# Optimization experiments

Hardware: AMD Instinct MI355X
Metric: run time of the kernel (lower is better)

The kernel has to match this reference:

```python
import jax, jax.numpy as jnp
import numpy as np

B, OBS, ACT, H, K = 32768, 64, 12, 256, 16
LOG_STD_MIN, LOG_STD_MAX = -10.0, 2.0


def setup_inputs() -> dict:
    key = jax.random.key(0)
    ks = jax.random.split(key, 9)
    s = lambda k, shape, scale: jax.random.normal(k, shape, jnp.float32) * scale
    return {
        "obs": jax.random.normal(ks[0], (B, OBS), jnp.float32),
        "idx": jax.random.randint(ks[1], (B,), 0, K),
        "noise": jax.random.normal(ks[2], (B, ACT), jnp.float32),
        "W1": s(ks[3], (OBS, H), 0.1), "b1": jnp.zeros((H,), jnp.float32),
        "W2": s(ks[4], (H, H), 0.05), "b2": jnp.zeros((H,), jnp.float32),
        "HW1": s(ks[5], (K, H, H), 0.05), "Hb1": jnp.zeros((K, H), jnp.float32),
        "HW2": s(ks[6], (K, H, 2 * ACT), 0.05), "Hb2": jnp.zeros((K, 2 * ACT), jnp.float32),
    }


def reference(obs, idx, noise, W1, b1, W2, b2, HW1, Hb1, HW2, Hb2):
    # Trunk MLP: Linear-ReLU-Linear, then the Sequential's extra ReLU.
    h = jax.nn.relu(obs @ W1 + b1)
    h = h @ W2 + b2
    h = jax.nn.relu(h)  # [B, H]
    # Per-head ensemble FFN computed densely for ALL heads (as in the original).
    y = jax.nn.relu(jnp.einsum('bh,khd->kbd', h, HW1) + Hb1[:, None, :])  # [K, B, H]
    out = jnp.einsum('kbd,kde->kbe', y, HW2) + Hb2[:, None, :]            # [K, B, 2A]
    # Top-1 per-sample head gather: out[idx, arange(B)]
    out = out[idx, jnp.arange(obs.shape[0])]                              # [B, 2A]
    A = out.shape[-1] // 2
    mean, log_std = out[:, :A], out[:, A:]
    # Bounded std via tanh
    log_std = LOG_STD_MIN + 0.5 * (LOG_STD_MAX - LOG_STD_MIN) * (jnp.tanh(log_std) + 1.0)
    std = jnp.exp(log_std)
    # rsample with explicit noise
    act = mean + std * noise
    # Normal log_prob
    logp = -0.5 * jnp.square((act - mean) / std) - log_std - 0.5 * jnp.log(2.0 * jnp.pi)
    # tanh squash with log-det correction
    sq = jnp.tanh(act)
    slogp = jnp.sum(logp - jnp.log(1.0 - jnp.square(sq) + 1e-6), axis=-1)  # [B]
    return sq, slogp
```

## Files before the change

### kernel.cpp

```cpp
#include <hip/hip_runtime.h>
#include <hip/hip_bf16.h>

typedef __bf16 bf16x8 __attribute__((ext_vector_type(8)));
typedef float  f32x4  __attribute__((ext_vector_type(4)));

#define MFMA16(a,b,c) __builtin_amdgcn_mfma_f32_16x16x32_bf16((a),(b),(c),0,0,0)

#define NB 32768

#define WS_COUNTS   0
#define WS_CURSORS  64
#define WS_TILEBASE 128
#define WS_BASES    256
#define WS_PERM     512
#define WS_W1P      131584
#define WS_W2P      164352
#define WS_HW1P     295424
#define WS_HW2P     2392576

__global__ void pack_kernel(const float* __restrict__ W1, const float* __restrict__ W2,
                            const float* __restrict__ HW1, const float* __restrict__ HW2,
                            char* __restrict__ ws) {
  if (blockIdx.x == 0 && threadIdx.x < 32)
    ((int*)ws)[threadIdx.x] = 0;
  int p = blockIdx.x * 256 + threadIdx.x;
  if (p < 16384) {
    int pp = p;
    int w = pp >> 12, r = pp & 4095;
    int f = r >> 9, e = r & 511;
    int lane = e >> 3, j = e & 7;
    int kt = f >> 2, nt = f & 3;
    int k = kt*32 + (lane>>4)*8 + j;
    int n = w*64 + nt*16 + (lane&15);
    ((__bf16*)(ws + WS_W1P))[pp] = (__bf16)W1[k*256 + n];
  } else if (p < 81920) {
    int pp = p - 16384;
    int w = pp >> 14, r = pp & 16383;
    int f = r >> 9, e = r & 511;
    int lane = e >> 3, j = e & 7;
    int kt = f >> 2, nt = f & 3;
    int k = kt*32 + (lane>>4)*8 + j;
    int n = w*64 + nt*16 + (lane&15);
    ((__bf16*)(ws + WS_W2P))[pp] = (__bf16)W2[k*256 + n];
  } else if (p < 1130496) {
    int p3 = p - 81920;
    int head = p3 >> 16, pp = p3 & 65535;
    int w = pp >> 14, r = pp & 16383;
    int f = r >> 9, e = r & 511;
    int lane = e >> 3, j = e & 7;
    int kt = f >> 2, nt = f & 3;
    int k = kt*32 + (lane>>4)*8 + j;
    int n = w*64 + nt*16 + (lane&15);
    ((__bf16*)(ws + WS_HW1P))[head*65536 + pp] = (__bf16)HW1[head*65536 + k*256 + n];
  } else if (p < 1261568) {
    int p4 = p - 1130496;
    int head = p4 >> 13, pp = p4 & 8191;
    int f = pp >> 9, e = pp & 511;
    int lane = e >> 3, j = e & 7;
    int kt = f >> 1, nt = f & 1;
    int k = kt*32 + (lane>>4)*8 + j;
    int n = nt*16 + (lane&15);
    __bf16 v = (__bf16)0.0f;
    if (n < 24) v = (__bf16)HW2[head*(256*24) + k*24 + n];
    ((__bf16*)(ws + WS_HW2P))[head*8192 + pp] = v;
  }
}

__global__ void hist_kernel(const int* __restrict__ idx, char* __restrict__ ws) {
  __shared__ int lc[16];
  int t = threadIdx.x;
  if (t < 16) lc[t] = 0;
  __syncthreads();
  int b = blockIdx.x * 256 + t;
  atomicAdd(&lc[idx[b]], 1);
  __syncthreads();
  if (t < 16 && lc[t]) atomicAdd(&((int*)(ws + WS_COUNTS))[t], lc[t]);
}

__global__ void scan_kernel(char* __restrict__ ws) {
  if (threadIdx.x == 0) {
    int* counts  = (int*)(ws + WS_COUNTS);
    int* cursors = (int*)(ws + WS_CURSORS);
    int* tb      = (int*)(ws + WS_TILEBASE);
    int* bases   = (int*)(ws + WS_BASES);
    int base = 0, tbase = 0;
    for (int k = 0; k < 16; k++) {
      bases[k] = base; cursors[k] = base; tb[k] = tbase;
      base  += counts[k];
      tbase += (counts[k] + 63) >> 6;
    }
    tb[16] = tbase;
  }
}

__global__ void scatter_kernel(const int* __restrict__ idx, char* __restrict__ ws) {
  __shared__ int lc[16], lbase[16];
  int t = threadIdx.x;
  if (t < 16) lc[t] = 0;
  __syncthreads();
  int b = blockIdx.x * 256 + t;
  int k = idx[b];
  int lp = atomicAdd(&lc[k], 1);
  __syncthreads();
  if (t < 16 && lc[t]) lbase[t] = atomicAdd(&((int*)(ws + WS_CURSORS))[t], lc[t]);
  __syncthreads();
  ((int*)(ws + WS_PERM))[lbase[k] + lp] = b;
}

__device__ __forceinline__ void gemm_relu(char* sA, const __bf16* __restrict__ Bp,
                                          const float* __restrict__ bias, int w, int l) {
  int q = l >> 4, l15 = l & 15;
  f32x4 zf = {0.f, 0.f, 0.f, 0.f};
  f32x4 acc[4][4];
#pragma unroll
  for (int mt = 0; mt < 4; mt++)
#pragma unroll
    for (int nt = 0; nt < 4; nt++) acc[mt][nt] = zf;
#pragma unroll
  for (int kt = 0; kt < 8; kt++) {
    bf16x8 af[4], bg[4];
#pragma unroll
    for (int mt = 0; mt < 4; mt++)
      af[mt] = *(const bf16x8*)(sA + (mt*16 + l15)*528 + (kt*32 + q*8)*2);
#pragma unroll
    for (int nt = 0; nt < 4; nt++)
      bg[nt] = *(const bf16x8*)(Bp + w*16384 + (kt*4 + nt)*512 + l*8);
#pragma unroll
    for (int mt = 0; mt < 4; mt++)
#pragma unroll
      for (int nt = 0; nt < 4; nt++)
        acc[mt][nt] = MFMA16(af[mt], bg[nt], acc[mt][nt]);
  }
  __syncthreads();
  float bv[4];
#pragma unroll
  for (int nt = 0; nt < 4; nt++) bv[nt] = bias[w*64 + nt*16 + l15];
#pragma unroll
  for (int mt = 0; mt < 4; mt++)
#pragma unroll
    for (int nt = 0; nt < 4; nt++)
#pragma unroll
      for (int r = 0; r < 4; r++) {
        float v = fmaxf(acc[mt][nt][r] + bv[nt], 0.f);
        int row = mt*16 + q*4 + r;
        int col = w*64 + nt*16 + l15;
        *(__bf16*)(sA + row*528 + col*2) = (__bf16)v;
      }
  __syncthreads();
}

__global__ __launch_bounds__(256, 2)
void actor_kernel(const float* __restrict__ obs, const float* __restrict__ noise,
                  const float* __restrict__ b1, const float* __restrict__ b2,
                  const float* __restrict__ Hb1, const float* __restrict__ Hb2,
                  const char* __restrict__ ws, float* __restrict__ out) {
  __shared__ __align__(16) char smem[43264];
  char*  sA    = smem;
  char*  sA0   = smem + 33792;
  float* souts = (float*)(smem + 33792);
  int*   rows  = (int*)(smem + 43008);

  const int* cnts  = (const int*)(ws + WS_COUNTS);
  const int* tb    = (const int*)(ws + WS_TILEBASE);
  const int* bases = (const int*)(ws + WS_BASES);
  const int* perm  = (const int*)(ws + WS_PERM);

  int bid = blockIdx.x;
  if (bid >= tb[16]) return;
  int head = 0;
#pragma unroll
  for (int k = 1; k < 16; k++) if (bid >= tb[k]) head = k;
  int row0  = bases[head] + (bid - tb[head]) * 64;
  int nrows = bases[head] + cnts[head] - row0;
  if (nrows > 64) nrows = 64;

  int t = threadIdx.x;
  int w = t >> 6, l = t & 63, q = l >> 4, l15 = l & 15;

  if (t < 64) rows[t] = (t < nrows) ? perm[row0 + t] : -1;
  __syncthreads();

  for (int s = t; s < 512; s += 256) {
    int m = s >> 3, c = (s & 7) << 3;
    int rm = rows[m];
    bf16x8 v = {};
    if (rm >= 0) {
#pragma unroll
      for (int i = 0; i < 8; i++) v[i] = (__bf16)obs[rm*64 + c + i];
    }
    *(bf16x8*)(sA0 + m*144 + c*2) = v;
  }
  __syncthreads();

  {
    const __bf16* Bp = (const __bf16*)(ws + WS_W1P) + w*4096;
    f32x4 zf = {0.f, 0.f, 0.f, 0.f};
    f32x4 acc[4][4];
#pragma unroll
    for (int mt = 0; mt < 4; mt++)
#pragma unroll
      for (int nt = 0; nt < 4; nt++) acc[mt][nt] = zf;
#pragma unroll
    for (int kt = 0; kt < 2; kt++) {
      bf16x8 af[4], bg[4];
#pragma unroll
      for (int mt = 0; mt < 4; mt++)
        af[mt] = *(const bf16x8*)(sA0 + (mt*16 + l15)*144 + (kt*32 + q*8)*2);
#pragma unroll
      for (int nt = 0; nt < 4; nt++)
        bg[nt] = *(const bf16x8*)(Bp + (kt*4 + nt)*512 + l*8);
#pragma unroll
      for (int mt = 0; mt < 4; mt++)
#pragma unroll
        for (int nt = 0; nt < 4; nt++)
          acc[mt][nt] = MFMA16(af[mt], bg[nt], acc[mt][nt]);
    }
    float bv[4];
#pragma unroll
    for (int nt = 0; nt < 4; nt++) bv[nt] = b1[w*64 + nt*16 + l15];
#pragma unroll
    for (int mt = 0; mt < 4; mt++)
#pragma unroll
      for (int nt = 0; nt < 4; nt++)
#pragma unroll
        for (int r = 0; r < 4; r++) {
          float v = fmaxf(acc[mt][nt][r] + bv[nt], 0.f);
          int row = mt*16 + q*4 + r;
          int col = w*64 + nt*16 + l15;
          *(__bf16*)(sA + row*528 + col*2) = (__bf16)v;
        }
  }
  __syncthreads();

  gemm_relu(sA, (const __bf16*)(ws + WS_W2P), b2, w, l);
  gemm_relu(sA, (const __bf16*)(ws + WS_HW1P) + head*65536, Hb1 + head*256, w, l);

  {
    const __bf16* Bp = (const __bf16*)(ws + WS_HW2P) + head*8192;
    f32x4 zf = {0.f, 0.f, 0.f, 0.f};
    f32x4 c4[2]; c4[0] = zf; c4[1] = zf;
#pragma unroll
    for (int kt = 0; kt < 8; kt++) {
      bf16x8 af = *(const bf16x8*)(sA + (w*16 + l15)*528 + (kt*32 + q*8)*2);
#pragma unroll
      for (int nt = 0; nt < 2; nt++) {
        bf16x8 bg = *(const bf16x8*)(Bp + (kt*2 + nt)*512 + l*8);
        c4[nt] = MFMA16(af, bg, c4[nt]);
      }
    }
    __syncthreads();
#pragma unroll
    for (int nt = 0; nt < 2; nt++)
#pragma unroll
      for (int r = 0; r < 4; r++) {
        int row = w*16 + q*4 + r;
        int col = nt*16 + l15;
        float v = c4[nt][r];
        if (col < 24) v += Hb2[head*24 + col];
        souts[row*32 + col] = v;
      }
  }
  __syncthreads();

  {
    int row = t >> 2, sub = t & 3;
    int bnum = (row < nrows) ? rows[row] : -1;
    float s = 0.f;
    if (bnum >= 0) {
#pragma unroll
      for (int i = 0; i < 3; i++) {
        int a = sub*3 + i;
        float mean = souts[row*32 + a];
        float lsr  = souts[row*32 + 12 + a];
        float ls   = -10.f + 6.f*(tanhf(lsr) + 1.f);
        float sd   = __expf(ls);
        float nz   = noise[bnum*12 + a];
        float act  = mean + sd*nz;
        float sq   = tanhf(act);
        out[bnum*12 + a] = sq;
        s += -0.5f*nz*nz - ls - 0.91893853320467274f - __logf(1.f - sq*sq + 1e-6f);
      }
    }
    s += __shfl_xor(s, 1);
    s += __shfl_xor(s, 2);
    if (bnum >= 0 && sub == 0) out[NB*12 + bnum] = s;
  }
}

extern "C" void kernel_launch(void* const* d_in, const int* in_sizes, int n_in,
                              void* d_out, int out_size, void* d_ws, size_t ws_size,
                              hipStream_t stream) {
  const float* obs   = (const float*)d_in[0];
  const int*   idx   = (const int*)d_in[1];
  const float* noise = (const float*)d_in[2];
  const float* W1    = (const float*)d_in[3];
  const float* b1    = (const float*)d_in[4];
  const float* W2    = (const float*)d_in[5];
  const float* b2    = (const float*)d_in[6];
  const float* HW1   = (const float*)d_in[7];
  const float* Hb1   = (const float*)d_in[8];
  const float* HW2   = (const float*)d_in[9];
  const float* Hb2   = (const float*)d_in[10];
  char* ws = (char*)d_ws;

  pack_kernel<<<4928, 256, 0, stream>>>(W1, W2, HW1, HW2, ws);
  hist_kernel<<<128, 256, 0, stream>>>(idx, ws);
  scan_kernel<<<1, 64, 0, stream>>>(ws);
  scatter_kernel<<<128, 256, 0, stream>>>(idx, ws);
  actor_kernel<<<528, 256, 0, stream>>>(obs, noise, b1, b2, Hb1, Hb2, ws, (float*)d_out);
}
```

Before: 108.4 us.

## Drop histogram and scan kernels via per-head bucket scatter; tile weight packing

Removes the hist and scan launches. Each head now gets a fixed-capacity bucket in the permutation buffer, and the scatter cursors serve directly as per-head counts, which the actor kernel reads to compute its tile-to-head mapping. The weight pack kernel is rewritten to stage 32-row slabs through shared memory with coalesced float4 reads and vectorized bf16x8 writes, using far fewer blocks. This costs a larger workspace of 16 buckets times 32768 ints and adds a 16-entry prefix loop in every actor block.

```diff
diff --git a/kernel.cpp b/kernel.cpp
--- a/kernel.cpp
+++ b/kernel.cpp
@@ -7,89 +7,67 @@
 #define MFMA16(a,b,c) __builtin_amdgcn_mfma_f32_16x16x32_bf16((a),(b),(c),0,0,0)
 
 #define NB 32768
-
-#define WS_COUNTS   0
+#define CAP 32768
+
 #define WS_CURSORS  64
-#define WS_TILEBASE 128
-#define WS_BASES    256
 #define WS_PERM     512
-#define WS_W1P      131584
-#define WS_W2P      164352
-#define WS_HW1P     295424
-#define WS_HW2P     2392576
-
-__global__ void pack_kernel(const float* __restrict__ W1, const float* __restrict__ W2,
-                            const float* __restrict__ HW1, const float* __restrict__ HW2,
-                            char* __restrict__ ws) {
-  if (blockIdx.x == 0 && threadIdx.x < 32)
-    ((int*)ws)[threadIdx.x] = 0;
-  int p = blockIdx.x * 256 + threadIdx.x;
-  if (p < 16384) {
-    int pp = p;
-    int w = pp >> 12, r = pp & 4095;
-    int f = r >> 9, e = r & 511;
-    int lane = e >> 3, j = e & 7;
-    int kt = f >> 2, nt = f & 3;
-    int k = kt*32 + (lane>>4)*8 + j;
-    int n = w*64 + nt*16 + (lane&15);
-    ((__bf16*)(ws + WS_W1P))[pp] = (__bf16)W1[k*256 + n];
-  } else if (p < 81920) {
-    int pp = p - 16384;
-    int w = pp >> 14, r = pp & 16383;
-    int f = r >> 9, e = r & 511;
-    int lane = e >> 3, j = e & 7;
-    int kt = f >> 2, nt = f & 3;
-    int k = kt*32 + (lane>>4)*8 + j;
-    int n = w*64 + nt*16 + (lane&15);
-    ((__bf16*)(ws + WS_W2P))[pp] = (__bf16)W2[k*256 + n];
-  } else if (p < 1130496) {
-    int p3 = p - 81920;
-    int head = p3 >> 16, pp = p3 & 65535;
-    int w = pp >> 14, r = pp & 16383;
-    int f = r >> 9, e = r & 511;
-    int lane = e >> 3, j = e & 7;
-    int kt = f >> 2, nt = f & 3;
-    int k = kt*32 + (lane>>4)*8 + j;
-    int n = w*64 + nt*16 + (lane&15);
-    ((__bf16*)(ws + WS_HW1P))[head*65536 + pp] = (__bf16)HW1[head*65536 + k*256 + n];
-  } else if (p < 1261568) {
-    int p4 = p - 1130496;
-    int head = p4 >> 13, pp = p4 & 8191;
-    int f = pp >> 9, e = pp & 511;
-    int lane = e >> 3, j = e & 7;
-    int kt = f >> 1, nt = f & 1;
-    int k = kt*32 + (lane>>4)*8 + j;
-    int n = nt*16 + (lane&15);
-    __bf16 v = (__bf16)0.0f;
-    if (n < 24) v = (__bf16)HW2[head*(256*24) + k*24 + n];
-    ((__bf16*)(ws + WS_HW2P))[head*8192 + pp] = v;
-  }
-}
-
-__global__ void hist_kernel(const int* __restrict__ idx, char* __restrict__ ws) {
-  __shared__ int lc[16];
-  int t = threadIdx.x;
-  if (t < 16) lc[t] = 0;
-  __syncthreads();
-  int b = blockIdx.x * 256 + t;
-  atomicAdd(&lc[idx[b]], 1);
-  __syncthreads();
-  if (t < 16 && lc[t]) atomicAdd(&((int*)(ws + WS_COUNTS))[t], lc[t]);
-}
-
-__global__ void scan_kernel(char* __restrict__ ws) {
-  if (threadIdx.x == 0) {
-    int* counts  = (int*)(ws + WS_COUNTS);
-    int* cursors = (int*)(ws + WS_CURSORS);
-    int* tb      = (int*)(ws + WS_TILEBASE);
-    int* bases   = (int*)(ws + WS_BASES);
-    int base = 0, tbase = 0;
-    for (int k = 0; k < 16; k++) {
-      bases[k] = base; cursors[k] = base; tb[k] = tbase;
-      base  += counts[k];
-      tbase += (counts[k] + 63) >> 6;
-    }
-    tb[16] = tbase;
+#define WS_W1P      2097664
+#define WS_W2P      2130432
+#define WS_HW1P     2261504
+#define WS_HW2P     4358656
+
+__global__ __launch_bounds__(256)
+void pack_kernel(const float* __restrict__ W1, const float* __restrict__ W2,
+                 const float* __restrict__ HW1, const float* __restrict__ HW2,
+                 char* __restrict__ ws) {
+  __shared__ __bf16 tile[32 * 260];
+  int b = blockIdx.x, t = threadIdx.x;
+  if (b == 0 && t < 32) ((int*)ws)[t] = 0;
+
+  const float* src; __bf16* dst; int kt, wstride, hw2 = 0;
+  if (b < 2)        { src = W1;  dst = (__bf16*)(ws + WS_W1P); kt = b;      wstride = 4096;  }
+  else if (b < 10)  { src = W2;  dst = (__bf16*)(ws + WS_W2P); kt = b - 2;  wstride = 16384; }
+  else if (b < 138) { int h = (b - 10) >> 3; kt = (b - 10) & 7;
+                      src = HW1 + h*65536; dst = (__bf16*)(ws + WS_HW1P) + h*65536; wstride = 16384; }
+  else              { int h = (b - 138) >> 3; kt = (b - 138) & 7;
+                      src = HW2 + h*6144;  dst = (__bf16*)(ws + WS_HW2P) + h*8192;  hw2 = 1; }
+
+  int wv = t >> 6, l = t & 63;
+  if (!hw2) {
+    const float4* s4 = (const float4*)(src + kt*32*256);
+#pragma unroll
+    for (int p = 0; p < 8; p++) {
+      int i = p*256 + t;
+      int rr = i >> 6, c4 = i & 63;
+      float4 v = s4[i];
+      __bf16* d = &tile[rr*260 + c4*4];
+      d[0] = (__bf16)v.x; d[1] = (__bf16)v.y; d[2] = (__bf16)v.z; d[3] = (__bf16)v.w;
+    }
+    __syncthreads();
+#pragma unroll
+    for (int nt = 0; nt < 4; nt++) {
+      bf16x8 v;
+#pragma unroll
+      for (int j = 0; j < 8; j++)
+        v[j] = tile[((l>>4)*8 + j)*260 + wv*64 + nt*16 + (l&15)];
+      *(bf16x8*)(dst + wv*wstride + (kt*4 + nt)*512 + l*8) = v;
+    }
+  } else {
+    for (int s = t; s < 32*40; s += 256) tile[s] = (__bf16)0.f;
+    __syncthreads();
+    for (int s = t; s < 768; s += 256) {
+      float v = src[kt*768 + s];
+      int r = s / 24, c = s - r*24;
+      tile[r*40 + c] = (__bf16)v;
+    }
+    __syncthreads();
+    if (wv < 2) {
+      int nt = wv;
+      bf16x8 v;
+#pragma unroll
+      for (int j = 0; j < 8; j++) v[j] = tile[((l>>4)*8 + j)*40 + nt*16 + (l&15)];
+      *(bf16x8*)(dst + (kt*2 + nt)*512 + l*8) = v;
+    }
   }
 }
 
@@ -104,7 +82,7 @@
   __syncthreads();
   if (t < 16 && lc[t]) lbase[t] = atomicAdd(&((int*)(ws + WS_CURSORS))[t], lc[t]);
   __syncthreads();
-  ((int*)(ws + WS_PERM))[lbase[k] + lp] = b;
+  ((int*)(ws + WS_PERM))[k*CAP + lbase[k] + lp] = b;
 }
 
 __device__ __forceinline__ void gemm_relu(char* sA, const __bf16* __restrict__ Bp,
@@ -160,24 +138,27 @@
   float* souts = (float*)(smem + 33792);
   int*   rows  = (int*)(smem + 43008);
 
-  const int* cnts  = (const int*)(ws + WS_COUNTS);
-  const int* tb    = (const int*)(ws + WS_TILEBASE);
-  const int* bases = (const int*)(ws + WS_BASES);
-  const int* perm  = (const int*)(ws + WS_PERM);
+  const int* cur  = (const int*)(ws + WS_CURSORS);
+  const int* perm = (const int*)(ws + WS_PERM);
 
   int bid = blockIdx.x;
-  if (bid >= tb[16]) return;
-  int head = 0;
-#pragma unroll
-  for (int k = 1; k < 16; k++) if (bid >= tb[k]) head = k;
-  int row0  = bases[head] + (bid - tb[head]) * 64;
-  int nrows = bases[head] + cnts[head] - row0;
+  int accT = 0, head = -1, cnt = 0, tloc = 0;
+#pragma unroll
+  for (int k = 0; k < 16; k++) {
+    int c = cur[k];
+    int ntl = (c + 63) >> 6;
+    if (head < 0 && bid < accT + ntl) { head = k; tloc = bid - accT; cnt = c; }
+    accT += ntl;
+  }
+  if (head < 0) return;
+  int row0  = tloc * 64;
+  int nrows = cnt - row0;
   if (nrows > 64) nrows = 64;
 
   int t = threadIdx.x;
   int w = t >> 6, l = t & 63, q = l >> 4, l15 = l & 15;
 
-  if (t < 64) rows[t] = (t < nrows) ? perm[row0 + t] : -1;
+  if (t < 64) rows[t] = (t < nrows) ? perm[head*CAP + row0 + t] : -1;
   __syncthreads();
 
   for (int s = t; s < 512; s += 256) {
@@ -303,9 +284,7 @@
   const float* Hb2   = (const float*)d_in[10];
   char* ws = (char*)d_ws;
 
-  pack_kernel<<<4928, 256, 0, stream>>>(W1, W2, HW1, HW2, ws);
-  hist_kernel<<<128, 256, 0, stream>>>(idx, ws);
-  scan_kernel<<<1, 64, 0, stream>>>(ws);
+  pack_kernel<<<266, 256, 0, stream>>>(W1, W2, HW1, HW2, ws);
   scatter_kernel<<<128, 256, 0, stream>>>(idx, ws);
   actor_kernel<<<528, 256, 0, stream>>>(obs, noise, b1, b2, Hb1, Hb2, ws, (float*)d_out);
 }
```

Measured after the change: 105.2 us. 1.03x faster.
